# Optimization experiments

Hardware: AMD Instinct MI355X
Metric: run time of the kernel (lower is better)

Reference implementation:

```python
import jax, jax.numpy as jnp
import numpy as np

B, S = 8, 1024          # 8 prefill sequences of length 1024, packed
HIDDEN = 4096
NH, NKV, HD = 32, 8, 128  # q heads, kv heads, head_dim = hidden // NH
G = NH // NKV             # GQA group size
NUM_BLOCKS, BLOCK_SIZE = 1024, 16
ROPE_THETA = 10000.0


def _apply_rope(q, k, pos):
    # q: [T, NH, HD], k: [T, NKV, HD], pos: [T] int32 (NeoX half-split rotation)
    half = HD // 2
    inv_freq = 1.0 / (ROPE_THETA ** (jnp.arange(0, HD, 2, dtype=jnp.float32) / HD))  # [half]
    ang = pos.astype(jnp.float32)[:, None] * inv_freq  # [T, half]
    cos = jnp.cos(ang)[:, None, :]  # [T, 1, half]
    sin = jnp.sin(ang)[:, None, :]

    def rot(t):
        t1, t2 = t[..., :half], t[..., half:]
        return jnp.concatenate([t1 * cos - t2 * sin, t2 * cos + t1 * sin], axis=-1)

    return rot(q), rot(k)


def setup_inputs() -> dict:
    key = jax.random.key(0)
    k1, k2, k3 = jax.random.split(key, 3)
    T = B * S
    x = jax.random.normal(k1, (T, HIDDEN), dtype=jnp.float32)
    wqkv = jax.random.normal(k2, (HIDDEN, (NH + 2 * NKV) * HD), dtype=jnp.float32) * 0.02
    bqkv = jnp.zeros(((NH + 2 * NKV) * HD,), dtype=jnp.float32)
    wo = jax.random.normal(k3, (NH * HD, HIDDEN), dtype=jnp.float32) * 0.02
    pos_list = jnp.tile(jnp.arange(S, dtype=jnp.int32), B)  # per-token position in its sequence
    # contiguous block allocation: token i of the packed batch -> cache slot i
    slot_mapping = jnp.arange(T, dtype=jnp.int32)  # block = slot // BLOCK_SIZE, offset = slot % BLOCK_SIZE
    k_cache = jnp.zeros((NUM_BLOCKS, BLOCK_SIZE, NKV, HD), dtype=jnp.float32)
    v_cache = jnp.zeros((NUM_BLOCKS, BLOCK_SIZE, NKV, HD), dtype=jnp.float32)
    return {"x": x, "wqkv": wqkv, "bqkv": bqkv, "wo": wo,
            "pos_list": pos_list, "slot_mapping": slot_mapping,
            "k_cache": k_cache, "v_cache": v_cache}


def reference(x, wqkv, bqkv, wo, pos_list, slot_mapping, k_cache, v_cache):
    scale = HD ** -0.5
    T = x.shape[0]
    qkv = x @ wqkv + bqkv  # [T, (NH+2*NKV)*HD]
    q = qkv[:, : NH * HD].reshape(T, NH, HD)
    k = qkv[:, NH * HD: (NH + NKV) * HD].reshape(T, NKV, HD)
    v = qkv[:, (NH + NKV) * HD:].reshape(T, NKV, HD)
    q, k = _apply_rope(q, k, pos_list)

    # varlen causal flash attention over B equal-length sequences (GQA)
    qb = q.reshape(B, S, NKV, G, HD)
    kb = k.reshape(B, S, NKV, HD)
    vb = v.reshape(B, S, NKV, HD)
    scores = jnp.einsum('bqhgd,bkhd->bhgqk', qb, kb) * scale  # [B,NKV,G,S,S]
    causal = jnp.tril(jnp.ones((S, S), dtype=bool))
    scores = jnp.where(causal, scores, jnp.float32(-1e30))
    probs = jax.nn.softmax(scores, axis=-1)
    out = jnp.einsum('bhgqk,bkhd->bqhgd', probs, vb).reshape(T, NH * HD)
    out = out @ wo  # [T, HIDDEN]

    # vectorized _write_to_paged_cache: scatter each token's k/v into its slot
    kc = k_cache.reshape(-1, NKV, HD).at[slot_mapping].set(k).reshape(k_cache.shape)
    vc = v_cache.reshape(-1, NKV, HD).at[slot_mapping].set(v).reshape(v_cache.shape)
    return out, kc, vc
```

## Files before the change

kernel.cpp:

```cpp
#include <hip/hip_runtime.h>

typedef unsigned short u16;
typedef unsigned int   u32;
typedef __attribute__((ext_vector_type(8))) short short8;
typedef __attribute__((ext_vector_type(4))) float f32x4;
typedef __attribute__((ext_vector_type(16))) float f32x16;
typedef __attribute__((ext_vector_type(4))) u16   u16x4;

#define GLOAD16(gp, lp) __builtin_amdgcn_global_load_lds( \
    (const __attribute__((address_space(1))) void*)(gp),   \
    (__attribute__((address_space(3))) void*)(lp), 16, 0, 0)

__device__ __forceinline__ float bf2f(u16 u) {
  union { u32 i; float f; } v; v.i = ((u32)u) << 16; return v.f;
}
__device__ __forceinline__ u16 f2bf(float f) {
  union { float f; u32 i; } v; v.f = f;
  return (u16)((v.i + 0x7fffu + ((v.i >> 16) & 1u)) >> 16);
}

#define TTOK 8192
#define SLEN 1024
#define NBATCH 8
#define NHQ 32
#define NKVH 8
#define HDIM 128
#define QKVW 6144
#define HID 4096

__global__ void ap_copyf4(const f32x4* __restrict__ src, f32x4* __restrict__ dst, int n4) {
  int stride = gridDim.x * 256;
  for (int i = blockIdx.x * 256 + threadIdx.x; i < n4; i += stride) dst[i] = src[i];
}

__global__ void ap_convx(const float* __restrict__ x, u16* __restrict__ xb) {
  size_t e = ((size_t)blockIdx.x * 256 + threadIdx.x) * 8;
  f32x4 a = *(const f32x4*)(x + e);
  f32x4 b = *(const f32x4*)(x + e + 4);
  short8 o;
  o[0]=(short)f2bf(a[0]); o[1]=(short)f2bf(a[1]); o[2]=(short)f2bf(a[2]); o[3]=(short)f2bf(a[3]);
  o[4]=(short)f2bf(b[0]); o[5]=(short)f2bf(b[1]); o[6]=(short)f2bf(b[2]); o[7]=(short)f2bf(b[3]);
  *(short8*)(xb + e) = o;
}

__global__ __launch_bounds__(256) void ap_tconv(const float* __restrict__ src,
                                                u16* __restrict__ dst, int K, int N) {
  __shared__ u16 tile[64][68];
  int nt = N >> 6;
  int tn = blockIdx.x % nt, tk = blockIdx.x / nt;
  int rr = threadIdx.x >> 4, cc = (threadIdx.x & 15) * 4;
#pragma unroll
  for (int i = 0; i < 4; ++i) {
    int row = i * 16 + rr;
    f32x4 v = *(const f32x4*)(src + (size_t)(tk * 64 + row) * N + tn * 64 + cc);
#pragma unroll
    for (int j = 0; j < 4; ++j) tile[row][cc + j] = f2bf(v[j]);
  }
  __syncthreads();
#pragma unroll
  for (int i = 0; i < 4; ++i) {
    int orow = i * 16 + rr;
    u16x4 o;
#pragma unroll
    for (int j = 0; j < 4; ++j) o[j] = tile[cc + j][orow];
    *(u16x4*)(dst + (size_t)(tn * 64 + orow) * K + tk * 64 + cc) = o;
  }
}

__device__ __forceinline__ void ap_stage(const u16* __restrict__ g, int ldk,
                                         u16* __restrict__ l, int tid) {
#pragma unroll
  for (int i = 0; i < 4; ++i) {
    int ci = i * 512 + tid;
    int r = ci >> 3;
    int cb = (ci & 7) * 16;
    int c = (cb ^ ((r & 7) << 4)) >> 1;
    GLOAD16(g + (size_t)r * ldk + c, l + ci * 8);
  }
}
__device__ __forceinline__ void ap_stage_half(const u16* __restrict__ g, int ldk,
                                              u16* __restrict__ l, int tid, int half) {
#pragma unroll
  for (int i = 0; i < 2; ++i) {
    int ci = half * 1024 + i * 512 + tid;
    int r = ci >> 3;
    int cb = (ci & 7) * 16;
    int c = (cb ^ ((r & 7) << 4)) >> 1;
    GLOAD16(g + (size_t)r * ldk + c, l + ci * 8);
  }
}

__device__ __forceinline__ short8 ds_frag(const u16* base, int row, int kbyte, int swz) {
  return *(const short8*)((const char*)base + row * 128 + (kbyte ^ swz));
}

template <int OUT_BF16, int HAS_BIAS>
__global__ __launch_bounds__(512, 2) void ap_gemm32(const u16* __restrict__ A,
                                                    const u16* __restrict__ BT,
                                                    const float* __restrict__ bias,
                                                    void* __restrict__ Cout,
                                                    int M, int N, int K, int nbn) {
  __shared__ u16 sA[2][16384];
  __shared__ u16 sB[2][16384];
  const int tid = threadIdx.x;
  const int wave = tid >> 6, l = tid & 63;
  const int l31 = l & 31, hi = l >> 5;
  const int wr = wave >> 2, wc = wave & 3;
  const int swz = (l & 7) << 4;

  const int nwg = nbn * (M >> 8);
  const int cpx = nwg >> 3;
  const int wg = (blockIdx.x & 7) * cpx + (blockIdx.x >> 3);
  const int bm = wg / nbn, bn = wg % nbn;

  f32x16 acc[4][2];
#pragma unroll
  for (int mf = 0; mf < 4; ++mf)
#pragma unroll
    for (int nf = 0; nf < 2; ++nf)
#pragma unroll
      for (int r = 0; r < 16; ++r) acc[mf][nf][r] = 0.f;

  const u16* Abase = A + (size_t)(bm * 256) * K;
  const u16* Bbase = BT + (size_t)(bn * 256) * K;
  const int NT = K >> 6;

  ap_stage(Abase, K, sA[0], tid);
  ap_stage(Bbase, K, sB[0], tid);

  for (int kt = 0; kt < NT; ++kt) {
    const u16* sAc = sA[kt & 1];
    const u16* sBc = sB[kt & 1];
    u16* sBn = sB[(kt + 1) & 1];
    const bool pf = (kt + 1 < NT);

    if (pf) {
      ap_stage(Abase + (kt + 1) * 64, K, sA[(kt + 1) & 1], tid);
      asm volatile("s_waitcnt vmcnt(4)" ::: "memory");
    } else {
      asm volatile("s_waitcnt vmcnt(0)" ::: "memory");
    }
    __builtin_amdgcn_s_barrier();
    __builtin_amdgcn_sched_barrier(0);

    short8 b0_[2][2], a0_[4][2], b1_[2][2], a1_[4][2];
#pragma unroll
    for (int nf = 0; nf < 2; ++nf)
#pragma unroll
      for (int ks = 0; ks < 2; ++ks)
        b0_[nf][ks] = ds_frag(sBc, wc * 64 + nf * 32 + l31, ks * 32 + hi * 16, swz);
#pragma unroll
    for (int mf = 0; mf < 4; ++mf)
#pragma unroll
      for (int ks = 0; ks < 2; ++ks)
        a0_[mf][ks] = ds_frag(sAc, wr * 128 + mf * 32 + l31, ks * 32 + hi * 16, swz);
    __builtin_amdgcn_sched_barrier(0);
#pragma unroll
    for (int nf = 0; nf < 2; ++nf)
#pragma unroll
      for (int ks = 0; ks < 2; ++ks)
        b1_[nf][ks] = ds_frag(sBc, wc * 64 + nf * 32 + l31, (ks + 2) * 32 + hi * 16, swz);
#pragma unroll
    for (int mf = 0; mf < 4; ++mf)
#pragma unroll
      for (int ks = 0; ks < 2; ++ks)
        a1_[mf][ks] = ds_frag(sAc, wr * 128 + mf * 32 + l31, (ks + 2) * 32 + hi * 16, swz);
    if (pf) ap_stage_half(Bbase + (kt + 1) * 64, K, sBn, tid, 0);

    asm volatile("s_waitcnt lgkmcnt(12)" ::: "memory");
    __builtin_amdgcn_sched_barrier(0);
    __builtin_amdgcn_s_setprio(1);
#pragma unroll
    for (int ks = 0; ks < 2; ++ks)
#pragma unroll
      for (int mf = 0; mf < 4; ++mf)
#pragma unroll
        for (int nf = 0; nf < 2; ++nf)
          acc[mf][nf] = __builtin_amdgcn_mfma_f32_32x32x16_bf16(
              a0_[mf][ks], b0_[nf][ks], acc[mf][nf], 0, 0, 0);
    __builtin_amdgcn_s_setprio(0);
    if (pf) ap_stage_half(Bbase + (kt + 1) * 64, K, sBn, tid, 1);

    asm volatile("s_waitcnt lgkmcnt(0)" ::: "memory");
    __builtin_amdgcn_sched_barrier(0);
    __builtin_amdgcn_s_barrier();
    __builtin_amdgcn_s_setprio(1);
#pragma unroll
    for (int ks = 0; ks < 2; ++ks)
#pragma unroll
      for (int mf = 0; mf < 4; ++mf)
#pragma unroll
        for (int nf = 0; nf < 2; ++nf)
          acc[mf][nf] = __builtin_amdgcn_mfma_f32_32x32x16_bf16(
              a1_[mf][ks], b1_[nf][ks], acc[mf][nf], 0, 0, 0);
    __builtin_amdgcn_s_setprio(0);
  }

#pragma unroll
  for (int mf = 0; mf < 4; ++mf)
#pragma unroll
    for (int nf = 0; nf < 2; ++nf) {
      int col = bn * 256 + wc * 64 + nf * 32 + l31;
      float bv = HAS_BIAS ? bias[col] : 0.f;
#pragma unroll
      for (int r = 0; r < 16; ++r) {
        int row = bm * 256 + wr * 128 + mf * 32 + (r & 3) + 8 * (r >> 2) + 4 * hi;
        float v = acc[mf][nf][r] + bv;
        if (OUT_BF16)
          ((u16*)Cout)[(size_t)row * N + col] = f2bf(v);
        else
          ((float*)Cout)[(size_t)row * N + col] = v;
      }
    }
}

__global__ __launch_bounds__(256) void ap_rope(u16* __restrict__ qkv,
                                               const int* __restrict__ pos_list,
                                               const int* __restrict__ slot_mapping,
                                               float* __restrict__ kc) {
  int gid = blockIdx.x * 4 + (threadIdx.x >> 6);
  int i = threadIdx.x & 63;
  int t = gid / 40, head = gid % 40;
  float pos = (float)pos_list[t];
  float inv = expf(-(float)i * 0.14391156516151135f);
  float ang = pos * inv;
  float cs = cosf(ang), sn = sinf(ang);
  int cb = (head < 32) ? head * 128 : 4096 + (head - 32) * 128;
  u16* p = qkv + (size_t)t * QKVW + cb;
  float t1 = bf2f(p[i]), t2 = bf2f(p[i + 64]);
  float o1 = t1 * cs - t2 * sn;
  float o2 = t2 * cs + t1 * sn;
  p[i] = f2bf(o1);
  p[i + 64] = f2bf(o2);
  if (head >= 32) {
    int slot = slot_mapping[t];
    float* kp = kc + (size_t)slot * (NKVH * HDIM) + (head - 32) * 128;
    kp[i] = o1;
    kp[i + 64] = o2;
  }
}

__global__ void ap_vscatter(const u16* __restrict__ qkv,
                            const int* __restrict__ slot_mapping,
                            float* __restrict__ vc) {
  int idx = blockIdx.x * 256 + threadIdx.x;
  int e = idx * 4;
  int t = e >> 10, r = e & 1023;
  int slot = slot_mapping[t];
  u16x4 v = *(const u16x4*)(qkv + (size_t)t * QKVW + 5120 + r);
  f32x4 o;
#pragma unroll
  for (int j = 0; j < 4; ++j) o[j] = bf2f(v[j]);
  *(f32x4*)(vc + (size_t)slot * 1024 + r) = o;
}

__global__ __launch_bounds__(256) void ap_vtrans(const u16* __restrict__ qkv,
                                                 u16* __restrict__ Vt) {
  __shared__ u16 tile[64][68];
  int bid = blockIdx.x;
  int hdt = bid & 1, st = (bid >> 1) & 15, head = bid >> 5;
  int b = head >> 3, h = head & 7;
  int rr = threadIdx.x >> 4, cc = (threadIdx.x & 15) * 4;
#pragma unroll
  for (int i = 0; i < 4; ++i) {
    int s = i * 16 + rr;
    u16x4 v = *(const u16x4*)(qkv + (size_t)(b * 1024 + st * 64 + s) * QKVW + 5120 +
                              h * 128 + hdt * 64 + cc);
#pragma unroll
    for (int j = 0; j < 4; ++j) tile[s][cc + j] = v[j];
  }
  __syncthreads();
#pragma unroll
  for (int i = 0; i < 4; ++i) {
    int hd = i * 16 + rr;
    u16x4 o;
#pragma unroll
    for (int j = 0; j < 4; ++j) o[j] = tile[cc + j][hd];
    *(u16x4*)(Vt + (size_t)head * (HDIM * SLEN) + (size_t)(hdt * 64 + hd) * SLEN +
              st * 64 + cc) = o;
  }
}

__global__ __launch_bounds__(512) void ap_attn4(const u16* __restrict__ qkv,
                                                const u16* __restrict__ Vt,
                                                u16* __restrict__ O) {
  __shared__ u16 sK[64 * 136];
  __shared__ u16 sV[128 * 72];
  __shared__ u16 sP[8 * 32 * 72];
  const int tid = threadIdx.x;
  const int wave = tid >> 6, l = tid & 63, l16 = l & 15, lq = l >> 4;
  const int bid = blockIdx.x;
  const int qt = bid & 15;
  const int kvh = (bid >> 4) & 7;
  const int b = bid >> 7;
  const int qh = kvh * 4 + (wave & 3);
  const int q0 = qt * 64 + (wave >> 2) * 32;
  const int head = b * 8 + kvh;
  const float SC2 = 0.12751649736230717f;

  short8 qf[2][4];
#pragma unroll
  for (int m = 0; m < 2; ++m)
#pragma unroll
    for (int kd = 0; kd < 4; ++kd) {
      size_t t = (size_t)(b * 1024 + q0 + m * 16 + l16);
      qf[m][kd] = *(const short8*)(qkv + t * QKVW + qh * 128 + kd * 32 + lq * 8);
    }

  u16* sPw = sP + wave * 2304;
  f32x4 zv = {0.f, 0.f, 0.f, 0.f};
  f32x4 oacc[2][8];
#pragma unroll
  for (int m = 0; m < 2; ++m)
#pragma unroll
    for (int n = 0; n < 8; ++n) oacc[m][n] = zv;
  float mrun[2][4], lrun[2][4];
#pragma unroll
  for (int m = 0; m < 2; ++m)
#pragma unroll
    for (int r = 0; r < 4; ++r) { mrun[m][r] = -1e30f; lrun[m][r] = 0.f; }

  const int ntiles = qt + 1;
  for (int kt = 0; kt < ntiles; ++kt) {
    const int kv0 = kt * 64;
#pragma unroll
    for (int i = 0; i < 2; ++i) {
      int ci = i * 512 + tid;
      int kr = ci >> 4, ko = (ci & 15) * 8;
      short8 v = *(const short8*)(qkv + (size_t)(b * 1024 + kv0 + kr) * QKVW + 4096 +
                                  kvh * 128 + ko);
      *(short8*)&sK[kr * 136 + ko] = v;
    }
#pragma unroll
    for (int i = 0; i < 2; ++i) {
      int ci = i * 512 + tid;
      int hd = ci >> 3, ko = (ci & 7) * 8;
      short8 v = *(const short8*)(Vt + (size_t)head * (HDIM * SLEN) + (size_t)hd * SLEN +
                                  kv0 + ko);
      *(short8*)&sV[hd * 72 + ko] = v;
    }
    __syncthreads();

    f32x4 sacc[2][4];
#pragma unroll
    for (int m = 0; m < 2; ++m)
#pragma unroll
      for (int nf = 0; nf < 4; ++nf) sacc[m][nf] = zv;
#pragma unroll
    for (int kd = 0; kd < 4; ++kd) {
      short8 kf[4];
#pragma unroll
      for (int nf = 0; nf < 4; ++nf)
        kf[nf] = *(const short8*)&sK[(nf * 16 + l16) * 136 + kd * 32 + lq * 8];
#pragma unroll
      for (int m = 0; m < 2; ++m)
#pragma unroll
        for (int nf = 0; nf < 4; ++nf)
          sacc[m][nf] = __builtin_amdgcn_mfma_f32_16x16x32_bf16(qf[m][kd], kf[nf], sacc[m][nf], 0, 0, 0);
    }
    if (kv0 + 63 > q0) {
#pragma unroll
      for (int m = 0; m < 2; ++m)
#pragma unroll
        for (int nf = 0; nf < 4; ++nf) {
          int kv = kv0 + nf * 16 + l16;
#pragma unroll
          for (int r = 0; r < 4; ++r) {
            int q = q0 + m * 16 + lq * 4 + r;
            if (kv > q) sacc[m][nf][r] = -1e30f;
          }
        }
    }
#pragma unroll
    for (int m = 0; m < 2; ++m)
#pragma unroll
      for (int r = 0; r < 4; ++r) {
        float mx = fmaxf(fmaxf(sacc[m][0][r], sacc[m][1][r]),
                         fmaxf(sacc[m][2][r], sacc[m][3][r]));
#pragma unroll
        for (int off = 8; off; off >>= 1) mx = fmaxf(mx, __shfl_xor(mx, off));
        float mn = fmaxf(mrun[m][r], mx);
        float sc = exp2f((mrun[m][r] - mn) * SC2);
        mrun[m][r] = mn;
        float p0 = exp2f((sacc[m][0][r] - mn) * SC2);
        float p1 = exp2f((sacc[m][1][r] - mn) * SC2);
        float p2 = exp2f((sacc[m][2][r] - mn) * SC2);
        float p3 = exp2f((sacc[m][3][r] - mn) * SC2);
        float rs = (p0 + p1) + (p2 + p3);
#pragma unroll
        for (int off = 8; off; off >>= 1) rs += __shfl_xor(rs, off);
        lrun[m][r] = lrun[m][r] * sc + rs;
#pragma unroll
        for (int n = 0; n < 8; ++n) oacc[m][n][r] *= sc;
        int prow = (m * 16 + lq * 4 + r) * 72;
        sPw[prow + l16]      = f2bf(p0);
        sPw[prow + 16 + l16] = f2bf(p1);
        sPw[prow + 32 + l16] = f2bf(p2);
        sPw[prow + 48 + l16] = f2bf(p3);
      }
    short8 pa[2][2];
#pragma unroll
    for (int m = 0; m < 2; ++m)
#pragma unroll
      for (int ks = 0; ks < 2; ++ks)
        pa[m][ks] = *(const short8*)&sPw[(m * 16 + l16) * 72 + ks * 32 + lq * 8];
#pragma unroll
    for (int n = 0; n < 8; ++n) {
#pragma unroll
      for (int ks = 0; ks < 2; ++ks) {
        short8 vb = *(const short8*)&sV[(n * 16 + l16) * 72 + ks * 32 + lq * 8];
#pragma unroll
        for (int m = 0; m < 2; ++m)
          oacc[m][n] = __builtin_amdgcn_mfma_f32_16x16x32_bf16(pa[m][ks], vb, oacc[m][n], 0, 0, 0);
      }
    }
    __syncthreads();
  }
#pragma unroll
  for (int m = 0; m < 2; ++m)
#pragma unroll
    for (int r = 0; r < 4; ++r) {
      float inv = 1.f / lrun[m][r];
      size_t t = (size_t)(b * 1024 + q0 + m * 16 + lq * 4 + r);
#pragma unroll
      for (int n = 0; n < 8; ++n)
        O[t * (size_t)HID + qh * 128 + n * 16 + l16] = f2bf(oacc[m][n][r] * inv);
    }
}

extern "C" void kernel_launch(void* const* d_in, const int* in_sizes, int n_in,
                              void* d_out, int out_size, void* d_ws, size_t ws_size,
                              hipStream_t stream) {
  const float* x = (const float*)d_in[0];
  const float* wqkv = (const float*)d_in[1];
  const float* bqkv = (const float*)d_in[2];
  const float* wo = (const float*)d_in[3];
  const int* pos_list = (const int*)d_in[4];
  const int* slot_mapping = (const int*)d_in[5];
  const float* k_cache = (const float*)d_in[6];
  const float* v_cache = (const float*)d_in[7];

  float* out = (float*)d_out;
  float* kc = out + (size_t)33554432;
  float* vc = kc + (size_t)16777216;

  char* ws = (char*)d_ws;
  u16* xb    = (u16*)(ws);
  u16* wqkvT = (u16*)(ws + 67108864);
  u16* woT   = (u16*)(ws + 117440512);
  u16* qkvb  = (u16*)(ws + 150994944);
  u16* Vt    = (u16*)(ws + 251658240);
  u16* attnO = xb;

  ap_copyf4<<<4096, 256, 0, stream>>>((const f32x4*)k_cache, (f32x4*)kc, 4194304);
  ap_copyf4<<<4096, 256, 0, stream>>>((const f32x4*)v_cache, (f32x4*)vc, 4194304);
  ap_convx<<<16384, 256, 0, stream>>>(x, xb);
  ap_tconv<<<6144, 256, 0, stream>>>(wqkv, wqkvT, 4096, 6144);
  ap_tconv<<<4096, 256, 0, stream>>>(wo, woT, 4096, 4096);
  ap_gemm32<1, 1><<<768, 512, 0, stream>>>(xb, wqkvT, bqkv, qkvb, 8192, 6144, 4096, 24);
  ap_rope<<<81920, 256, 0, stream>>>(qkvb, pos_list, slot_mapping, kc);
  ap_vscatter<<<8192, 256, 0, stream>>>(qkvb, slot_mapping, vc);
  ap_vtrans<<<2048, 256, 0, stream>>>(qkvb, Vt);
  ap_attn4<<<1024, 512, 0, stream>>>(qkvb, Vt, attnO);
  ap_gemm32<0, 0><<<512, 512, 0, stream>>>(attnO, woT, nullptr, out, 8192, 4096, 4096, 16);
}
```

Before: 1.185 ms.

## Rewrite projection GEMMs with 16 waves and 16x16x32 MFMA tiles

Replaces the 512-thread GEMM built on 32x32x16 MFMA with a 1024-thread variant. In the new kernel each of 16 waves computes a 64x64 sub-tile using 16x16x32 bf16 MFMA with 4x4 f32x4 accumulators. Staging of A and B for the next k-tile is now issued up front together, and the split half-prefetch of B interleaved with compute is removed. The intent is more waves to hide latency and fewer registers per thread, at the cost of one occupancy slot per CU (64 KB LDS, 1024 threads), less overlap of loads with MFMA, and smaller MFMA shapes with lower per-instruction reuse.

```diff
diff --git a/kernel.cpp b/kernel.cpp
--- a/kernel.cpp
+++ b/kernel.cpp
@@ -4,7 +4,6 @@
 typedef unsigned int   u32;
 typedef __attribute__((ext_vector_type(8))) short short8;
 typedef __attribute__((ext_vector_type(4))) float f32x4;
-typedef __attribute__((ext_vector_type(16))) float f32x16;
 typedef __attribute__((ext_vector_type(4))) u16   u16x4;
 
 #define GLOAD16(gp, lp) __builtin_amdgcn_global_load_lds( \
@@ -67,75 +66,62 @@
   }
 }
 
-__device__ __forceinline__ void ap_stage(const u16* __restrict__ g, int ldk,
-                                         u16* __restrict__ l, int tid) {
-#pragma unroll
-  for (int i = 0; i < 4; ++i) {
-    int ci = i * 512 + tid;
+__device__ __forceinline__ void ap_stage1k(const u16* __restrict__ g, int ldk,
+                                           u16* __restrict__ l, int tid) {
+#pragma unroll
+  for (int i = 0; i < 2; ++i) {
+    int ci = i * 1024 + tid;
     int r = ci >> 3;
     int cb = (ci & 7) * 16;
     int c = (cb ^ ((r & 7) << 4)) >> 1;
     GLOAD16(g + (size_t)r * ldk + c, l + ci * 8);
   }
 }
-__device__ __forceinline__ void ap_stage_half(const u16* __restrict__ g, int ldk,
-                                              u16* __restrict__ l, int tid, int half) {
-#pragma unroll
-  for (int i = 0; i < 2; ++i) {
-    int ci = half * 1024 + i * 512 + tid;
-    int r = ci >> 3;
-    int cb = (ci & 7) * 16;
-    int c = (cb ^ ((r & 7) << 4)) >> 1;
-    GLOAD16(g + (size_t)r * ldk + c, l + ci * 8);
-  }
-}
 
 __device__ __forceinline__ short8 ds_frag(const u16* base, int row, int kbyte, int swz) {
   return *(const short8*)((const char*)base + row * 128 + (kbyte ^ swz));
 }
 
 template <int OUT_BF16, int HAS_BIAS>
-__global__ __launch_bounds__(512, 2) void ap_gemm32(const u16* __restrict__ A,
-                                                    const u16* __restrict__ BT,
-                                                    const float* __restrict__ bias,
-                                                    void* __restrict__ Cout,
-                                                    int M, int N, int K, int nbn) {
+__global__ __launch_bounds__(1024) void ap_gemmw(const u16* __restrict__ A,
+                                                 const u16* __restrict__ BT,
+                                                 const float* __restrict__ bias,
+                                                 void* __restrict__ Cout,
+                                                 int M, int N, int K, int nbn) {
   __shared__ u16 sA[2][16384];
   __shared__ u16 sB[2][16384];
   const int tid = threadIdx.x;
-  const int wave = tid >> 6, l = tid & 63;
-  const int l31 = l & 31, hi = l >> 5;
+  const int wave = tid >> 6, l = tid & 63, l16 = l & 15, lq = l >> 4;
   const int wr = wave >> 2, wc = wave & 3;
-  const int swz = (l & 7) << 4;
+  const int swz = (l16 & 7) << 4;
 
   const int nwg = nbn * (M >> 8);
   const int cpx = nwg >> 3;
   const int wg = (blockIdx.x & 7) * cpx + (blockIdx.x >> 3);
   const int bm = wg / nbn, bn = wg % nbn;
 
-  f32x16 acc[4][2];
+  f32x4 acc[4][4];
+  f32x4 zv = {0.f, 0.f, 0.f, 0.f};
 #pragma unroll
   for (int mf = 0; mf < 4; ++mf)
 #pragma unroll
-    for (int nf = 0; nf < 2; ++nf)
-#pragma unroll
-      for (int r = 0; r < 16; ++r) acc[mf][nf][r] = 0.f;
+    for (int nf = 0; nf < 4; ++nf) acc[mf][nf] = zv;
 
   const u16* Abase = A + (size_t)(bm * 256) * K;
   const u16* Bbase = BT + (size_t)(bn * 256) * K;
   const int NT = K >> 6;
 
-  ap_stage(Abase, K, sA[0], tid);
-  ap_stage(Bbase, K, sB[0], tid);
+  ap_stage1k(Abase, K, sA[0], tid);
+  ap_stage1k(Bbase, K, sB[0], tid);
 
   for (int kt = 0; kt < NT; ++kt) {
     const u16* sAc = sA[kt & 1];
     const u16* sBc = sB[kt & 1];
-    u16* sBn = sB[(kt + 1) & 1];
     const bool pf = (kt + 1 < NT);
 
     if (pf) {
-      ap_stage(Abase + (kt + 1) * 64, K, sA[(kt + 1) & 1], tid);
+      ap_stage1k(Abase + (kt + 1) * 64, K, sA[(kt + 1) & 1], tid);
+      ap_stage1k(Bbase + (kt + 1) * 64, K, sB[(kt + 1) & 1], tid);
       asm volatile("s_waitcnt vmcnt(4)" ::: "memory");
     } else {
       asm volatile("s_waitcnt vmcnt(0)" ::: "memory");
@@ -143,68 +129,56 @@
     __builtin_amdgcn_s_barrier();
     __builtin_amdgcn_sched_barrier(0);
 
-    short8 b0_[2][2], a0_[4][2], b1_[2][2], a1_[4][2];
-#pragma unroll
-    for (int nf = 0; nf < 2; ++nf)
-#pragma unroll
-      for (int ks = 0; ks < 2; ++ks)
-        b0_[nf][ks] = ds_frag(sBc, wc * 64 + nf * 32 + l31, ks * 32 + hi * 16, swz);
-#pragma unroll
-    for (int mf = 0; mf < 4; ++mf)
-#pragma unroll
-      for (int ks = 0; ks < 2; ++ks)
-        a0_[mf][ks] = ds_frag(sAc, wr * 128 + mf * 32 + l31, ks * 32 + hi * 16, swz);
-    __builtin_amdgcn_sched_barrier(0);
-#pragma unroll
-    for (int nf = 0; nf < 2; ++nf)
-#pragma unroll
-      for (int ks = 0; ks < 2; ++ks)
-        b1_[nf][ks] = ds_frag(sBc, wc * 64 + nf * 32 + l31, (ks + 2) * 32 + hi * 16, swz);
-#pragma unroll
-    for (int mf = 0; mf < 4; ++mf)
-#pragma unroll
-      for (int ks = 0; ks < 2; ++ks)
-        a1_[mf][ks] = ds_frag(sAc, wr * 128 + mf * 32 + l31, (ks + 2) * 32 + hi * 16, swz);
-    if (pf) ap_stage_half(Bbase + (kt + 1) * 64, K, sBn, tid, 0);
-
-    asm volatile("s_waitcnt lgkmcnt(12)" ::: "memory");
-    __builtin_amdgcn_sched_barrier(0);
-    __builtin_amdgcn_s_setprio(1);
-#pragma unroll
-    for (int ks = 0; ks < 2; ++ks)
+    {
+      short8 bf_[4], af_[4];
+#pragma unroll
+      for (int nf = 0; nf < 4; ++nf)
+        bf_[nf] = ds_frag(sBc, wc * 64 + nf * 16 + l16, lq * 16, swz);
 #pragma unroll
       for (int mf = 0; mf < 4; ++mf)
-#pragma unroll
-        for (int nf = 0; nf < 2; ++nf)
-          acc[mf][nf] = __builtin_amdgcn_mfma_f32_32x32x16_bf16(
-              a0_[mf][ks], b0_[nf][ks], acc[mf][nf], 0, 0, 0);
-    __builtin_amdgcn_s_setprio(0);
-    if (pf) ap_stage_half(Bbase + (kt + 1) * 64, K, sBn, tid, 1);
-
-    asm volatile("s_waitcnt lgkmcnt(0)" ::: "memory");
-    __builtin_amdgcn_sched_barrier(0);
-    __builtin_amdgcn_s_barrier();
-    __builtin_amdgcn_s_setprio(1);
-#pragma unroll
-    for (int ks = 0; ks < 2; ++ks)
+        af_[mf] = ds_frag(sAc, wr * 64 + mf * 16 + l16, lq * 16, swz);
+      asm volatile("s_waitcnt lgkmcnt(0)" ::: "memory");
+      __builtin_amdgcn_sched_barrier(0);
+      __builtin_amdgcn_s_setprio(1);
 #pragma unroll
       for (int mf = 0; mf < 4; ++mf)
 #pragma unroll
-        for (int nf = 0; nf < 2; ++nf)
-          acc[mf][nf] = __builtin_amdgcn_mfma_f32_32x32x16_bf16(
-              a1_[mf][ks], b1_[nf][ks], acc[mf][nf], 0, 0, 0);
-    __builtin_amdgcn_s_setprio(0);
+        for (int nf = 0; nf < 4; ++nf)
+          acc[mf][nf] = __builtin_amdgcn_mfma_f32_16x16x32_bf16(
+              af_[mf], bf_[nf], acc[mf][nf], 0, 0, 0);
+      __builtin_amdgcn_s_setprio(0);
+    }
+    {
+      short8 bf_[4], af_[4];
+#pragma unroll
+      for (int nf = 0; nf < 4; ++nf)
+        bf_[nf] = ds_frag(sBc, wc * 64 + nf * 16 + l16, 64 + lq * 16, swz);
+#pragma unroll
+      for (int mf = 0; mf < 4; ++mf)
+        af_[mf] = ds_frag(sAc, wr * 64 + mf * 16 + l16, 64 + lq * 16, swz);
+      asm volatile("s_waitcnt lgkmcnt(0)" ::: "memory");
+      __builtin_amdgcn_sched_barrier(0);
+      __builtin_amdgcn_s_barrier();
+      __builtin_amdgcn_s_setprio(1);
+#pragma unroll
+      for (int mf = 0; mf < 4; ++mf)
+#pragma unroll
+        for (int nf = 0; nf < 4; ++nf)
+          acc[mf][nf] = __builtin_amdgcn_mfma_f32_16x16x32_bf16(
+              af_[mf], bf_[nf], acc[mf][nf], 0, 0, 0);
+      __builtin_amdgcn_s_setprio(0);
+    }
   }
 
 #pragma unroll
   for (int mf = 0; mf < 4; ++mf)
 #pragma unroll
-    for (int nf = 0; nf < 2; ++nf) {
-      int col = bn * 256 + wc * 64 + nf * 32 + l31;
+    for (int nf = 0; nf < 4; ++nf) {
+      int col = bn * 256 + wc * 64 + nf * 16 + l16;
       float bv = HAS_BIAS ? bias[col] : 0.f;
 #pragma unroll
-      for (int r = 0; r < 16; ++r) {
-        int row = bm * 256 + wr * 128 + mf * 32 + (r & 3) + 8 * (r >> 2) + 4 * hi;
+      for (int r = 0; r < 4; ++r) {
+        int row = bm * 256 + wr * 64 + mf * 16 + lq * 4 + r;
         float v = acc[mf][nf][r] + bv;
         if (OUT_BF16)
           ((u16*)Cout)[(size_t)row * N + col] = f2bf(v);
@@ -457,10 +431,10 @@
   ap_convx<<<16384, 256, 0, stream>>>(x, xb);
   ap_tconv<<<6144, 256, 0, stream>>>(wqkv, wqkvT, 4096, 6144);
   ap_tconv<<<4096, 256, 0, stream>>>(wo, woT, 4096, 4096);
-  ap_gemm32<1, 1><<<768, 512, 0, stream>>>(xb, wqkvT, bqkv, qkvb, 8192, 6144, 4096, 24);
+  ap_gemmw<1, 1><<<768, 1024, 0, stream>>>(xb, wqkvT, bqkv, qkvb, 8192, 6144, 4096, 24);
   ap_rope<<<81920, 256, 0, stream>>>(qkvb, pos_list, slot_mapping, kc);
   ap_vscatter<<<8192, 256, 0, stream>>>(qkvb, slot_mapping, vc);
   ap_vtrans<<<2048, 256, 0, stream>>>(qkvb, Vt);
   ap_attn4<<<1024, 512, 0, stream>>>(qkvb, Vt, attnO);
-  ap_gemm32<0, 0><<<512, 512, 0, stream>>>(attnO, woT, nullptr, out, 8192, 4096, 4096, 16);
-}
+  ap_gemmw<0, 0><<<512, 1024, 0, stream>>>(attnO, woT, nullptr, out, 8192, 4096, 4096, 16);
+}
```

Measured after the change: 1.139 ms. -3.9%, faster.
